# Optimization experiments

Measured on AMD Instinct MI355X. Metric: run time of the kernel, lower is better.

Reference implementation:

```python
import jax, jax.numpy as jnp
import numpy as np

B, C, H, W, NCH = 2, 256, 48, 48, 12


def setup_inputs() -> dict:
    key = jax.random.key(0)
    k1, k2, k3, k4, k5 = jax.random.split(key, 5)
    gray_feature = jax.random.normal(k1, (B, C, H, W), jnp.float32)
    rgb_feature = jax.random.normal(k2, (B, C, H, W), jnp.float32)
    rgb_image = jax.random.uniform(k3, (B, 3, H, W), jnp.float32)
    # one-hot segmentation labels: random class id per pixel in [0, NCH)
    gcls = jax.random.randint(k4, (B, H, W), 0, NCH)
    rcls = jax.random.randint(k5, (B, H, W), 0, NCH)
    gray_label = jax.nn.one_hot(gcls, NCH, axis=1, dtype=jnp.float32)
    rgb_label = jax.nn.one_hot(rcls, NCH, axis=1, dtype=jnp.float32)
    return dict(gray_feature=gray_feature, rgb_feature=rgb_feature,
                rgb_image=rgb_image, gray_label=gray_label, rgb_label=rgb_label)


def _masked_normalize(feat, maskf):
    # feat: [b,c,N], maskf: [b,N] in {0,1}. Subtract per-channel masked mean,
    # then divide each masked pixel's feature vector by its channel-norm.
    cnt = maskf.sum(-1)                                            # [b]
    mean = jnp.einsum('bcn,bn->bc', feat, maskf) / jnp.maximum(cnt, 1.0)[:, None]
    bar = (feat - mean[:, :, None]) * maskf[:, None, :]            # zero outside mask
    norm = jnp.sqrt(jnp.sum(bar * bar, axis=1))                    # [b,N]
    unit = bar / jnp.where(norm > 0, norm, 1.0)[:, None, :]
    return unit, cnt


def reference(gray_feature, rgb_feature, rgb_image, gray_label, rgb_label):
    b, c, h, w = gray_feature.shape
    N = h * w
    gf = gray_feature.reshape(b, c, N)
    rf = rgb_feature.reshape(b, c, N)
    img = rgb_image.reshape(b, 3, N)
    gms = gray_label.reshape(b, -1, N) > 0.5   # [b,NCH,N] bool
    rms = rgb_label.reshape(b, -1, N) > 0.5
    canvas = -jnp.ones((b, 3, N), gray_feature.dtype)
    NEG = jnp.asarray(-1e30, gray_feature.dtype)
    for k in range(1, 12):  # classes 1..11, matching the torch loop
        gm = gms[:, k]                                     # [b,N]
        rm = rms[:, k]
        gmf = gm.astype(gf.dtype)
        rmf = rm.astype(rf.dtype)
        gn, cg = _masked_normalize(gf, gmf)                # [b,c,N]
        rn, cr = _masked_normalize(rf, rmf)
        # normalized correlation between gray and rgb masked pixels
        corr = jnp.einsum('bci,bcj->bij', gn, rn)          # [b,N,N]
        logits = jnp.where(rm[:, None, :], corr, NEG)      # softmax over rgb-mask pixels
        sm = jax.nn.softmax(logits, axis=-1)
        out = jnp.einsum('bij,bcj->bci', sm, img)          # [b,3,N]
        # skip condition from torch: needs >=2 pixels on each side
        valid = (cg > 1) & (cr > 1)                        # [b]
        write = gm & valid[:, None]                        # [b,N]
        canvas = jnp.where(write[:, None, :], out, canvas)
    return canvas.reshape(b, 3, h, w)
```

## Files before the change

### kernel.cpp

```cpp
#include <hip/hip_runtime.h>
#include <math.h>

#define BN 2
#define CC 256
#define NN 2304
#define KK 12
#define MC 320
#define QT 16
#define KTL 256
#define KCH 32
#define BPAD 260
#define APAD 18
#define KB_ACT 11

#define OFF_CNT_G   0
#define OFF_CNT_R   32
#define OFF_IDX_G   64
#define OFF_CPS_G   (OFF_IDX_G + BN * KK * MC)
#define OFF_CPS_R   (OFF_CPS_G + BN * NN)
#define OFF_MSUM_G  (OFF_CPS_R + BN * NN)
#define OFF_MSUM_R  (OFF_MSUM_G + BN * KK * CC)
#define OFF_IMGC    (OFF_MSUM_R + BN * KK * CC)
#define OFF_INV_G   (OFF_IMGC + BN * KK * 3 * MC)
#define OFF_INV_R   (OFF_INV_G + BN * KK * MC)
#define OFF_UCG     (OFF_INV_R + BN * KK * MC)
#define OFF_UCR     (OFF_UCG + BN * KK * MC * CC)

__global__ __launch_bounds__(256) void prep_mean_kernel(
        const float* __restrict__ gf, const float* __restrict__ rf,
        const float* __restrict__ img, const float* __restrict__ gl,
        const float* __restrict__ rl, float* __restrict__ out,
        int* cnt_g, int* cnt_r, int* idx_g, int* cps_g, int* cps_r,
        float* imgc, float* inv_g, float* inv_r,
        float* msum_g, float* msum_r) {
    __shared__ int wcnt[4];
    __shared__ float wsum[4][4][KK];
    int bid = blockIdx.x, tid = threadIdx.x;
    int lane = tid & 63, wid = tid >> 6;

    if (bid < 48) {
        int type = bid / (BN * KK);
        int rem = bid % (BN * KK);
        int b = rem / KK, k = rem % KK;
        const float* lp = (type ? rl : gl) + ((size_t)(b * KK + k)) * NN;
        int* cps = type ? cps_r : cps_g;
        int* cnt = type ? cnt_r : cnt_g;
        int base = 0;
        for (int c0 = 0; c0 < NN; c0 += 256) {
            int i = c0 + tid;
            bool p = lp[i] > 0.5f;
            unsigned long long m = __ballot(p);
            int rank = __popcll(m & ((1ull << lane) - 1));
            if (lane == 0) wcnt[wid] = __popcll(m);
            __syncthreads();
            int pre = 0;
            for (int w = 0; w < wid; ++w) pre += wcnt[w];
            int tot = wcnt[0] + wcnt[1] + wcnt[2] + wcnt[3];
            if (p) {
                int pos = base + pre + rank;
                cps[b * NN + i] = (k << 16) | pos;
                if (pos < MC) {
                    if (type) {
                        for (int ch = 0; ch < 3; ++ch)
                            imgc[((b * KK + k) * 3 + ch) * MC + pos] =
                                img[((size_t)(b * 3 + ch)) * NN + i];
                    } else {
                        idx_g[(b * KK + k) * MC + pos] = i;
                    }
                }
            }
            base += tot;
            __syncthreads();
        }
        if (tid == 0) cnt[b * KK + k] = base;
        int start = base < MC ? base : MC;
        for (int pos = start + tid; pos < MC; pos += 256) {
            if (type) {
                for (int ch = 0; ch < 3; ++ch)
                    imgc[((b * KK + k) * 3 + ch) * MC + pos] = 0.f;
            } else {
                idx_g[(b * KK + k) * MC + pos] = 0;
            }
        }
        float* invc = type ? inv_r : inv_g;
        for (int pos = tid; pos < MC; pos += 256)
            invc[(b * KK + k) * MC + pos] = 0.f;
    } else {
        int u = bid - 48;
        if (u < 54) out[u * 256 + tid] = -1.0f;
        int type = u >> 7;
        int rem = u & 127;
        int b = rem >> 6, cg = rem & 63;
        const float* fb = (type ? rf : gf) + ((size_t)(b * CC + cg * 4)) * NN;
        const float* lab = (type ? rl : gl) + ((size_t)b) * KK * NN;
        float* msum = type ? msum_r : msum_g;

        float acc[4][KK];
        #pragma unroll
        for (int c = 0; c < 4; ++c)
            #pragma unroll
            for (int kk = 0; kk < KK; ++kk) acc[c][kk] = 0.f;
        for (int i = tid; i < NN; i += 256) {
            float lv[KK];
            #pragma unroll
            for (int kk = 0; kk < KK; ++kk) lv[kk] = lab[(size_t)kk * NN + i];
            #pragma unroll
            for (int c = 0; c < 4; ++c) {
                float v = fb[(size_t)c * NN + i];
                #pragma unroll
                for (int kk = 0; kk < KK; ++kk) acc[c][kk] += lv[kk] * v;
            }
        }
        #pragma unroll
        for (int c = 0; c < 4; ++c)
            #pragma unroll
            for (int kk = 0; kk < KK; ++kk) {
                #pragma unroll
                for (int o = 32; o; o >>= 1)
                    acc[c][kk] += __shfl_xor(acc[c][kk], o, 64);
            }
        if (lane == 0) {
            #pragma unroll
            for (int c = 0; c < 4; ++c)
                #pragma unroll
                for (int kk = 0; kk < KK; ++kk) wsum[wid][c][kk] = acc[c][kk];
        }
        __syncthreads();
        if (tid < 48) {
            int c = tid / KK, kk = tid % KK;
            float s = wsum[0][c][kk] + wsum[1][c][kk] + wsum[2][c][kk] + wsum[3][c][kk];
            msum[(b * KK + kk) * CC + cg * 4 + c] = s;
        }
    }
}

__global__ __launch_bounds__(256) void center_kernel(
        const float* __restrict__ gf, const float* __restrict__ rf,
        const int* __restrict__ cps_g, const int* __restrict__ cps_r,
        const int* __restrict__ cnt_g, const int* __restrict__ cnt_r,
        const float* __restrict__ msum_g, const float* __restrict__ msum_r,
        float* ucg, float* ucr, float* inv_g, float* inv_r) {
    const int PCH = NN / 32;
    int blk = blockIdx.x;
    int type = blk / (BN * PCH);
    int rem = blk % (BN * PCH);
    int b = rem / PCH, chunk = rem % PCH;
    int i0 = chunk * 32;
    const float* f = type ? rf : gf;
    const int* cps = type ? cps_r : cps_g;
    const int* cnt = type ? cnt_r : cnt_g;
    const float* msum = type ? msum_r : msum_g;
    float* uc = type ? ucr : ucg;
    float* invc = type ? inv_r : inv_g;

    __shared__ float lmean[KK * 257];
    __shared__ float tile[64 * 33];

    int tid = threadIdx.x;
    for (int x = tid; x < KK * CC; x += 256) {
        int k = x >> 8, c = x & 255;
        float cn = fmaxf((float)cnt[b * KK + k], 1.f);
        lmean[k * 257 + c] = msum[(b * KK + k) * CC + c] / cn;
    }
    int p = tid >> 3, q = tid & 7;
    int pl = tid & 31, cb = tid >> 5;
    int kcpos = cps[b * NN + i0 + p];
    int kc = kcpos >> 16, pos = kcpos & 0xFFFF;
    bool wr = pos < MC;
    float ss = 0.f;
    float* ub = uc + ((size_t)((b * KK + kc) * MC + (wr ? pos : MC - 1))) * CC;
    for (int cc = 0; cc < 4; ++cc) {
        __syncthreads();
        for (int j = 0; j < 8; ++j) {
            int c = cb * 8 + j;
            tile[c * 33 + pl] = f[((size_t)(b * CC + cc * 64 + c)) * NN + i0 + pl];
        }
        __syncthreads();
        #pragma unroll
        for (int h = 0; h < 2; ++h) {
            int c0 = q * 8 + h * 4;
            float4 v;
            v.x = tile[(c0 + 0) * 33 + p] - lmean[kc * 257 + cc * 64 + c0 + 0];
            v.y = tile[(c0 + 1) * 33 + p] - lmean[kc * 257 + cc * 64 + c0 + 1];
            v.z = tile[(c0 + 2) * 33 + p] - lmean[kc * 257 + cc * 64 + c0 + 2];
            v.w = tile[(c0 + 3) * 33 + p] - lmean[kc * 257 + cc * 64 + c0 + 3];
            ss += v.x * v.x + v.y * v.y + v.z * v.z + v.w * v.w;
            if (wr) *(float4*)&ub[cc * 64 + c0] = v;
        }
    }
    ss += __shfl_xor(ss, 1, 64);
    ss += __shfl_xor(ss, 2, 64);
    ss += __shfl_xor(ss, 4, 64);
    if (q == 0 && wr)
        invc[(b * KK + kc) * MC + pos] = (ss > 0.f) ? rsqrtf(ss) : 1.0f;
}

__global__ __launch_bounds__(512) void corr_out_kernel(
        const int* __restrict__ cnt_g, const int* __restrict__ cnt_r,
        const int* __restrict__ idx_g,
        const float* __restrict__ ucg, const float* __restrict__ ucr,
        const float* __restrict__ inv_g, const float* __restrict__ inv_r,
        const float* __restrict__ imgc, float* __restrict__ out) {
    const int TNQ = MC / QT;
    const int NWG = BN * KB_ACT * TNQ;
    int bid = blockIdx.x;
    int x = (bid & 7) * (NWG / 8) + (bid >> 3);
    int tq = x % TNQ;
    int rest = x / TNQ;
    int k = 1 + rest % KB_ACT;
    int b = rest / KB_ACT;
    int bk = b * KK + k;
    int cg_ = cnt_g[bk], cr_ = cnt_r[bk];
    if (cg_ <= 1 || cr_ <= 1) return;
    int Mg = min(cg_, MC), Mr = min(cr_, MC);
    int q0 = tq * QT;
    if (q0 >= Mg) return;
    int mrp = (Mr + 3) & ~3;

    __shared__ float Af[CC * APAD];
    __shared__ float Bs[KCH * BPAD];

    int tid = threadIdx.x;
    {
        int r = tid >> 5, c32 = tid & 31;
        int rowi = q0 + r; if (rowi > MC - 1) rowi = MC - 1;
        const float* rowA = ucg + ((size_t)(bk * MC + rowi)) * CC;
        float4 v0 = *(const float4*)&rowA[c32 * 8];
        float4 v1 = *(const float4*)&rowA[c32 * 8 + 4];
        Af[(c32 * 8 + 0) * APAD + r] = v0.x;
        Af[(c32 * 8 + 1) * APAD + r] = v0.y;
        Af[(c32 * 8 + 2) * APAD + r] = v0.z;
        Af[(c32 * 8 + 3) * APAD + r] = v0.w;
        Af[(c32 * 8 + 4) * APAD + r] = v1.x;
        Af[(c32 * 8 + 5) * APAD + r] = v1.y;
        Af[(c32 * 8 + 6) * APAD + r] = v1.z;
        Af[(c32 * 8 + 7) * APAD + r] = v1.w;
    }

    int wid = tid >> 6;
    int lane = tid & 63;
    int r0 = q0 + 2 * wid;
    int r0c = (r0 > MC - 1) ? MC - 1 : r0;
    int r1c = (r0 + 1 > MC - 1) ? MC - 1 : r0 + 1;
    float invi0 = inv_g[bk * MC + r0c];
    float invi1 = inv_g[bk * MC + r1c];
    const float* im0 = imgc + (bk * 3 + 0) * MC;
    const float* im1 = imgc + (bk * 3 + 1) * MC;
    const float* im2 = imgc + (bk * 3 + 2) * MC;
    const float* ivr = inv_r + bk * MC;
    float s[2] = {0.f, 0.f}, p0[2] = {0.f, 0.f}, p1[2] = {0.f, 0.f}, p2[2] = {0.f, 0.f};

    for (int k0 = 0; k0 < Mr; k0 += KTL) {
        float acc[2][4];
        #pragma unroll
        for (int xx = 0; xx < 2; ++xx)
            #pragma unroll
            for (int y = 0; y < 4; ++y) acc[xx][y] = 0.f;
        int lim = mrp - k0;

        for (int kcc = 0; kcc < CC; kcc += KCH) {
            __syncthreads();
            {
                int cj = tid & 7;
                int colg = tid >> 3;
                #pragma unroll
                for (int p8 = 0; p8 < 4; ++p8) {
                    int col = colg + p8 * 64;
                    if (col < lim) {
                        int colr = k0 + col; if (colr > MC - 1) colr = MC - 1;
                        float4 vb = *(const float4*)(ucr +
                            ((size_t)(bk * MC + colr)) * CC + kcc + cj * 4);
                        Bs[(cj * 4 + 0) * BPAD + col] = vb.x;
                        Bs[(cj * 4 + 1) * BPAD + col] = vb.y;
                        Bs[(cj * 4 + 2) * BPAD + col] = vb.z;
                        Bs[(cj * 4 + 3) * BPAD + col] = vb.w;
                    }
                }
            }
            __syncthreads();
            #pragma unroll
            for (int kk = 0; kk < KCH; ++kk) {
                float2 av = *(const float2*)&Af[(kcc + kk) * APAD + 2 * wid];
                float4 bv = *(const float4*)&Bs[kk * BPAD + lane * 4];
                acc[0][0] += av.x * bv.x; acc[0][1] += av.x * bv.y;
                acc[0][2] += av.x * bv.z; acc[0][3] += av.x * bv.w;
                acc[1][0] += av.y * bv.x; acc[1][1] += av.y * bv.y;
                acc[1][2] += av.y * bv.z; acc[1][3] += av.y * bv.w;
            }
        }
        int kbase = k0 + lane * 4; if (kbase > MC - 4) kbase = MC - 4;
        float4 w0 = *(const float4*)&im0[kbase];
        float4 w1 = *(const float4*)&im1[kbase];
        float4 w2 = *(const float4*)&im2[kbase];
        float4 vj = *(const float4*)&ivr[kbase];
        float wj0[4] = {w0.x, w0.y, w0.z, w0.w};
        float wj1[4] = {w1.x, w1.y, w1.z, w1.w};
        float wj2[4] = {w2.x, w2.y, w2.z, w2.w};
        float vjj[4] = {vj.x, vj.y, vj.z, vj.w};
        #pragma unroll
        for (int y = 0; y < 4; ++y) {
            int col = k0 + lane * 4 + y;
            bool ok = col < Mr;
            float e0 = ok ? __expf(acc[0][y] * invi0 * vjj[y]) : 0.f;
            float e1 = ok ? __expf(acc[1][y] * invi1 * vjj[y]) : 0.f;
            s[0] += e0; p0[0] += e0 * wj0[y]; p1[0] += e0 * wj1[y]; p2[0] += e0 * wj2[y];
            s[1] += e1; p0[1] += e1 * wj0[y]; p1[1] += e1 * wj1[y]; p2[1] += e1 * wj2[y];
        }
    }
    #pragma unroll
    for (int o = 1; o <= 32; o <<= 1) {
        #pragma unroll
        for (int xx = 0; xx < 2; ++xx) {
            s[xx]  += __shfl_xor(s[xx],  o, 64);
            p0[xx] += __shfl_xor(p0[xx], o, 64);
            p1[xx] += __shfl_xor(p1[xx], o, 64);
            p2[xx] += __shfl_xor(p2[xx], o, 64);
        }
    }
    if (lane == 0) {
        #pragma unroll
        for (int xx = 0; xx < 2; ++xx) {
            int row = q0 + 2 * wid + xx;
            if (row < Mg) {
                int gi = idx_g[bk * MC + row];
                float inv = 1.0f / s[xx];
                out[((size_t)(b * 3 + 0)) * NN + gi] = p0[xx] * inv;
                out[((size_t)(b * 3 + 1)) * NN + gi] = p1[xx] * inv;
                out[((size_t)(b * 3 + 2)) * NN + gi] = p2[xx] * inv;
            }
        }
    }
}

extern "C" void kernel_launch(void* const* d_in, const int* in_sizes, int n_in,
                              void* d_out, int out_size, void* d_ws, size_t ws_size,
                              hipStream_t stream) {
    const float* gf  = (const float*)d_in[0];
    const float* rf  = (const float*)d_in[1];
    const float* img = (const float*)d_in[2];
    const float* gl  = (const float*)d_in[3];
    const float* rl  = (const float*)d_in[4];
    float* out = (float*)d_out;
    float* ws = (float*)d_ws;

    int*   cnt_g  = (int*)(ws + OFF_CNT_G);
    int*   cnt_r  = (int*)(ws + OFF_CNT_R);
    int*   idx_g  = (int*)(ws + OFF_IDX_G);
    int*   cps_g  = (int*)(ws + OFF_CPS_G);
    int*   cps_r  = (int*)(ws + OFF_CPS_R);
    float* msum_g = ws + OFF_MSUM_G;
    float* msum_r = ws + OFF_MSUM_R;
    float* imgc   = ws + OFF_IMGC;
    float* inv_g  = ws + OFF_INV_G;
    float* inv_r  = ws + OFF_INV_R;
    float* ucg    = ws + OFF_UCG;
    float* ucr    = ws + OFF_UCR;

    prep_mean_kernel<<<48 + 2 * BN * (CC / 4), 256, 0, stream>>>(
        gf, rf, img, gl, rl, out, cnt_g, cnt_r, idx_g, cps_g, cps_r,
        imgc, inv_g, inv_r, msum_g, msum_r);
    center_kernel<<<2 * BN * (NN / 32), 256, 0, stream>>>(
        gf, rf, cps_g, cps_r, cnt_g, cnt_r, msum_g, msum_r,
        ucg, ucr, inv_g, inv_r);
    corr_out_kernel<<<BN * KB_ACT * (MC / QT), 512, 0, stream>>>(
        cnt_g, cnt_r, idx_g, ucg, ucr, inv_g, inv_r, imgc, out);
}
```

Before: 113.8 us.

## Fuse three kernels into one cooperative persistent kernel with grid syncs

Combines the prep/mean, centering and correlation-softmax kernels into a single cooperative kernel of 256 blocks of 512 threads. The blocks loop over the former jobs and use grid.sync between phases instead of separate kernel launches. This removes the launch gaps between stages. In exchange it adds grid-wide barrier cost, reduces parallelism in the correlation phase (previously 440 blocks), and changes per-job thread mappings to suit 512-thread blocks.

```diff
diff --git a/kernel.cpp b/kernel.cpp
--- a/kernel.cpp
+++ b/kernel.cpp
@@ -1,5 +1,8 @@
 #include <hip/hip_runtime.h>
+#include <hip/hip_cooperative_groups.h>
 #include <math.h>
+
+namespace cg = cooperative_groups;
 
 #define BN 2
 #define CC 256
@@ -12,6 +15,8 @@
 #define BPAD 260
 #define APAD 18
 #define KB_ACT 11
+#define GRID 256
+#define BLK 512
 
 #define OFF_CNT_G   0
 #define OFF_CNT_R   32
@@ -26,307 +31,311 @@
 #define OFF_UCG     (OFF_INV_R + BN * KK * MC)
 #define OFF_UCR     (OFF_UCG + BN * KK * MC * CC)
 
-__global__ __launch_bounds__(256) void prep_mean_kernel(
+__global__ __launch_bounds__(BLK) void fused_kernel(
         const float* __restrict__ gf, const float* __restrict__ rf,
         const float* __restrict__ img, const float* __restrict__ gl,
         const float* __restrict__ rl, float* __restrict__ out,
-        int* cnt_g, int* cnt_r, int* idx_g, int* cps_g, int* cps_r,
-        float* imgc, float* inv_g, float* inv_r,
-        float* msum_g, float* msum_r) {
-    __shared__ int wcnt[4];
-    __shared__ float wsum[4][4][KK];
-    int bid = blockIdx.x, tid = threadIdx.x;
-    int lane = tid & 63, wid = tid >> 6;
-
-    if (bid < 48) {
-        int type = bid / (BN * KK);
-        int rem = bid % (BN * KK);
-        int b = rem / KK, k = rem % KK;
-        const float* lp = (type ? rl : gl) + ((size_t)(b * KK + k)) * NN;
-        int* cps = type ? cps_r : cps_g;
-        int* cnt = type ? cnt_r : cnt_g;
-        int base = 0;
-        for (int c0 = 0; c0 < NN; c0 += 256) {
-            int i = c0 + tid;
-            bool p = lp[i] > 0.5f;
-            unsigned long long m = __ballot(p);
-            int rank = __popcll(m & ((1ull << lane) - 1));
-            if (lane == 0) wcnt[wid] = __popcll(m);
-            __syncthreads();
-            int pre = 0;
-            for (int w = 0; w < wid; ++w) pre += wcnt[w];
-            int tot = wcnt[0] + wcnt[1] + wcnt[2] + wcnt[3];
-            if (p) {
-                int pos = base + pre + rank;
-                cps[b * NN + i] = (k << 16) | pos;
-                if (pos < MC) {
+        int* __restrict__ cnt_g, int* __restrict__ cnt_r,
+        int* __restrict__ idx_g, int* __restrict__ cps_g, int* __restrict__ cps_r,
+        float* __restrict__ imgc, float* __restrict__ inv_g, float* __restrict__ inv_r,
+        float* __restrict__ msum_g, float* __restrict__ msum_r,
+        float* __restrict__ ucg, float* __restrict__ ucr) {
+    cg::grid_group grid = cg::this_grid();
+    __shared__ float smem[CC * APAD + KCH * BPAD];
+
+    const int bid = blockIdx.x, tid = threadIdx.x;
+    const int lane = tid & 63, wid = tid >> 6;
+
+    {
+        int* wcnt = (int*)smem;
+        float* wsum = smem + 8;
+        for (int job = bid; job < 48 + 2 * BN * (CC / 4); job += GRID) {
+            if (job < 48) {
+                int type = job / (BN * KK);
+                int rem = job % (BN * KK);
+                int b = rem / KK, k = rem % KK;
+                const float* lp = (type ? rl : gl) + ((size_t)(b * KK + k)) * NN;
+                int* cps = type ? cps_r : cps_g;
+                int* cnt = type ? cnt_r : cnt_g;
+                int base = 0;
+                for (int c0 = 0; c0 < NN; c0 += BLK) {
+                    int i = c0 + tid;
+                    bool p = (i < NN) && (lp[i] > 0.5f);
+                    unsigned long long m = __ballot(p);
+                    int rank = __popcll(m & ((1ull << lane) - 1));
+                    if (lane == 0) wcnt[wid] = __popcll(m);
+                    __syncthreads();
+                    int pre = 0;
+                    for (int w = 0; w < wid; ++w) pre += wcnt[w];
+                    int tot = 0;
+                    for (int w = 0; w < 8; ++w) tot += wcnt[w];
+                    if (p) {
+                        int pos = base + pre + rank;
+                        cps[b * NN + i] = (k << 16) | pos;
+                        if (pos < MC) {
+                            if (type) {
+                                for (int ch = 0; ch < 3; ++ch)
+                                    imgc[((b * KK + k) * 3 + ch) * MC + pos] =
+                                        img[((size_t)(b * 3 + ch)) * NN + i];
+                            } else {
+                                idx_g[(b * KK + k) * MC + pos] = i;
+                            }
+                        }
+                    }
+                    base += tot;
+                    __syncthreads();
+                }
+                if (tid == 0) cnt[b * KK + k] = base;
+                int start = base < MC ? base : MC;
+                for (int pos = start + tid; pos < MC; pos += BLK) {
                     if (type) {
                         for (int ch = 0; ch < 3; ++ch)
-                            imgc[((b * KK + k) * 3 + ch) * MC + pos] =
-                                img[((size_t)(b * 3 + ch)) * NN + i];
+                            imgc[((b * KK + k) * 3 + ch) * MC + pos] = 0.f;
                     } else {
-                        idx_g[(b * KK + k) * MC + pos] = i;
-                    }
-                }
-            }
-            base += tot;
-            __syncthreads();
-        }
-        if (tid == 0) cnt[b * KK + k] = base;
-        int start = base < MC ? base : MC;
-        for (int pos = start + tid; pos < MC; pos += 256) {
-            if (type) {
-                for (int ch = 0; ch < 3; ++ch)
-                    imgc[((b * KK + k) * 3 + ch) * MC + pos] = 0.f;
+                        idx_g[(b * KK + k) * MC + pos] = 0;
+                    }
+                }
+                float* invc = type ? inv_r : inv_g;
+                for (int pos = tid; pos < MC; pos += BLK)
+                    invc[(b * KK + k) * MC + pos] = 0.f;
             } else {
-                idx_g[(b * KK + k) * MC + pos] = 0;
-            }
-        }
-        float* invc = type ? inv_r : inv_g;
-        for (int pos = tid; pos < MC; pos += 256)
-            invc[(b * KK + k) * MC + pos] = 0.f;
-    } else {
-        int u = bid - 48;
-        if (u < 54) out[u * 256 + tid] = -1.0f;
-        int type = u >> 7;
-        int rem = u & 127;
-        int b = rem >> 6, cg = rem & 63;
-        const float* fb = (type ? rf : gf) + ((size_t)(b * CC + cg * 4)) * NN;
-        const float* lab = (type ? rl : gl) + ((size_t)b) * KK * NN;
-        float* msum = type ? msum_r : msum_g;
-
-        float acc[4][KK];
-        #pragma unroll
-        for (int c = 0; c < 4; ++c)
-            #pragma unroll
-            for (int kk = 0; kk < KK; ++kk) acc[c][kk] = 0.f;
-        for (int i = tid; i < NN; i += 256) {
-            float lv[KK];
-            #pragma unroll
-            for (int kk = 0; kk < KK; ++kk) lv[kk] = lab[(size_t)kk * NN + i];
-            #pragma unroll
-            for (int c = 0; c < 4; ++c) {
-                float v = fb[(size_t)c * NN + i];
-                #pragma unroll
-                for (int kk = 0; kk < KK; ++kk) acc[c][kk] += lv[kk] * v;
-            }
-        }
-        #pragma unroll
-        for (int c = 0; c < 4; ++c)
-            #pragma unroll
-            for (int kk = 0; kk < KK; ++kk) {
-                #pragma unroll
-                for (int o = 32; o; o >>= 1)
-                    acc[c][kk] += __shfl_xor(acc[c][kk], o, 64);
-            }
-        if (lane == 0) {
-            #pragma unroll
-            for (int c = 0; c < 4; ++c)
-                #pragma unroll
-                for (int kk = 0; kk < KK; ++kk) wsum[wid][c][kk] = acc[c][kk];
-        }
-        __syncthreads();
-        if (tid < 48) {
-            int c = tid / KK, kk = tid % KK;
-            float s = wsum[0][c][kk] + wsum[1][c][kk] + wsum[2][c][kk] + wsum[3][c][kk];
-            msum[(b * KK + kk) * CC + cg * 4 + c] = s;
+                int u = job - 48;
+                if (u < 27) out[u * BLK + tid] = -1.0f;
+                int type = u >> 7;
+                int rem = u & 127;
+                int b = rem >> 6, cgq = rem & 63;
+                const float* fb = (type ? rf : gf) + ((size_t)(b * CC + cgq * 4)) * NN;
+                const float* lab = (type ? rl : gl) + ((size_t)b) * KK * NN;
+                float* msum = type ? msum_r : msum_g;
+
+                float acc[4][KK];
+                #pragma unroll
+                for (int c = 0; c < 4; ++c)
+                    #pragma unroll
+                    for (int kk = 0; kk < KK; ++kk) acc[c][kk] = 0.f;
+                for (int i = tid; i < NN; i += BLK) {
+                    float lv[KK];
+                    #pragma unroll
+                    for (int kk = 0; kk < KK; ++kk) lv[kk] = lab[(size_t)kk * NN + i];
+                    #pragma unroll
+                    for (int c = 0; c < 4; ++c) {
+                        float v = fb[(size_t)c * NN + i];
+                        #pragma unroll
+                        for (int kk = 0; kk < KK; ++kk) acc[c][kk] += lv[kk] * v;
+                    }
+                }
+                #pragma unroll
+                for (int c = 0; c < 4; ++c)
+                    #pragma unroll
+                    for (int kk = 0; kk < KK; ++kk) {
+                        #pragma unroll
+                        for (int o = 32; o; o >>= 1)
+                            acc[c][kk] += __shfl_xor(acc[c][kk], o, 64);
+                    }
+                if (lane == 0) {
+                    #pragma unroll
+                    for (int c = 0; c < 4; ++c)
+                        #pragma unroll
+                        for (int kk = 0; kk < KK; ++kk)
+                            wsum[(wid * 4 + c) * KK + kk] = acc[c][kk];
+                }
+                __syncthreads();
+                if (tid < 48) {
+                    int c = tid / KK, kk = tid % KK;
+                    float s = 0.f;
+                    for (int w = 0; w < 8; ++w) s += wsum[(w * 4 + c) * KK + kk];
+                    msum[(b * KK + kk) * CC + cgq * 4 + c] = s;
+                }
+            }
         }
     }
-}
-
-__global__ __launch_bounds__(256) void center_kernel(
-        const float* __restrict__ gf, const float* __restrict__ rf,
-        const int* __restrict__ cps_g, const int* __restrict__ cps_r,
-        const int* __restrict__ cnt_g, const int* __restrict__ cnt_r,
-        const float* __restrict__ msum_g, const float* __restrict__ msum_r,
-        float* ucg, float* ucr, float* inv_g, float* inv_r) {
-    const int PCH = NN / 32;
-    int blk = blockIdx.x;
-    int type = blk / (BN * PCH);
-    int rem = blk % (BN * PCH);
-    int b = rem / PCH, chunk = rem % PCH;
-    int i0 = chunk * 32;
-    const float* f = type ? rf : gf;
-    const int* cps = type ? cps_r : cps_g;
-    const int* cnt = type ? cnt_r : cnt_g;
-    const float* msum = type ? msum_r : msum_g;
-    float* uc = type ? ucr : ucg;
-    float* invc = type ? inv_r : inv_g;
-
-    __shared__ float lmean[KK * 257];
-    __shared__ float tile[64 * 33];
-
-    int tid = threadIdx.x;
-    for (int x = tid; x < KK * CC; x += 256) {
-        int k = x >> 8, c = x & 255;
-        float cn = fmaxf((float)cnt[b * KK + k], 1.f);
-        lmean[k * 257 + c] = msum[(b * KK + k) * CC + c] / cn;
-    }
-    int p = tid >> 3, q = tid & 7;
-    int pl = tid & 31, cb = tid >> 5;
-    int kcpos = cps[b * NN + i0 + p];
-    int kc = kcpos >> 16, pos = kcpos & 0xFFFF;
-    bool wr = pos < MC;
-    float ss = 0.f;
-    float* ub = uc + ((size_t)((b * KK + kc) * MC + (wr ? pos : MC - 1))) * CC;
-    for (int cc = 0; cc < 4; ++cc) {
-        __syncthreads();
-        for (int j = 0; j < 8; ++j) {
-            int c = cb * 8 + j;
-            tile[c * 33 + pl] = f[((size_t)(b * CC + cc * 64 + c)) * NN + i0 + pl];
-        }
-        __syncthreads();
-        #pragma unroll
-        for (int h = 0; h < 2; ++h) {
-            int c0 = q * 8 + h * 4;
-            float4 v;
-            v.x = tile[(c0 + 0) * 33 + p] - lmean[kc * 257 + cc * 64 + c0 + 0];
-            v.y = tile[(c0 + 1) * 33 + p] - lmean[kc * 257 + cc * 64 + c0 + 1];
-            v.z = tile[(c0 + 2) * 33 + p] - lmean[kc * 257 + cc * 64 + c0 + 2];
-            v.w = tile[(c0 + 3) * 33 + p] - lmean[kc * 257 + cc * 64 + c0 + 3];
-            ss += v.x * v.x + v.y * v.y + v.z * v.z + v.w * v.w;
-            if (wr) *(float4*)&ub[cc * 64 + c0] = v;
+    __threadfence();
+    grid.sync();
+
+    {
+        float* lmean = smem;
+        float* tile = smem + KK * 257;
+        const int PCH = NN / 32;
+        for (int job = bid; job < 2 * BN * PCH; job += GRID) {
+            __syncthreads();
+            int type = job / (BN * PCH);
+            int rem = job % (BN * PCH);
+            int b = rem / PCH, chunk = rem % PCH;
+            int i0 = chunk * 32;
+            const float* f = type ? rf : gf;
+            const int* cps = type ? cps_r : cps_g;
+            const int* cnt = type ? cnt_r : cnt_g;
+            const float* msum = type ? msum_r : msum_g;
+            float* uc = type ? ucr : ucg;
+            float* invc = type ? inv_r : inv_g;
+
+            for (int x = tid; x < KK * CC; x += BLK) {
+                int k = x >> 8, c = x & 255;
+                float cn = fmaxf((float)cnt[b * KK + k], 1.f);
+                lmean[k * 257 + c] = msum[(b * KK + k) * CC + c] / cn;
+            }
+            int p = tid >> 4, q = tid & 15;
+            int pl = tid & 31, cb = tid >> 5;
+            int kcpos = cps[b * NN + i0 + p];
+            int kc = kcpos >> 16, pos = kcpos & 0xFFFF;
+            bool wr = pos < MC;
+            float ss = 0.f;
+            float* ub = uc + ((size_t)((b * KK + kc) * MC + (wr ? pos : MC - 1))) * CC;
+            for (int cc = 0; cc < 4; ++cc) {
+                __syncthreads();
+                #pragma unroll
+                for (int j = 0; j < 4; ++j) {
+                    int c = cb * 4 + j;
+                    tile[c * 33 + pl] = f[((size_t)(b * CC + cc * 64 + c)) * NN + i0 + pl];
+                }
+                __syncthreads();
+                int c0 = q * 4;
+                float4 v;
+                v.x = tile[(c0 + 0) * 33 + p] - lmean[kc * 257 + cc * 64 + c0 + 0];
+                v.y = tile[(c0 + 1) * 33 + p] - lmean[kc * 257 + cc * 64 + c0 + 1];
+                v.z = tile[(c0 + 2) * 33 + p] - lmean[kc * 257 + cc * 64 + c0 + 2];
+                v.w = tile[(c0 + 3) * 33 + p] - lmean[kc * 257 + cc * 64 + c0 + 3];
+                ss += v.x * v.x + v.y * v.y + v.z * v.z + v.w * v.w;
+                if (wr) *(float4*)&ub[cc * 64 + c0] = v;
+            }
+            ss += __shfl_xor(ss, 1, 64);
+            ss += __shfl_xor(ss, 2, 64);
+            ss += __shfl_xor(ss, 4, 64);
+            ss += __shfl_xor(ss, 8, 64);
+            if (q == 0 && wr)
+                invc[(b * KK + kc) * MC + pos] = (ss > 0.f) ? rsqrtf(ss) : 1.0f;
         }
     }
-    ss += __shfl_xor(ss, 1, 64);
-    ss += __shfl_xor(ss, 2, 64);
-    ss += __shfl_xor(ss, 4, 64);
-    if (q == 0 && wr)
-        invc[(b * KK + kc) * MC + pos] = (ss > 0.f) ? rsqrtf(ss) : 1.0f;
-}
-
-__global__ __launch_bounds__(512) void corr_out_kernel(
-        const int* __restrict__ cnt_g, const int* __restrict__ cnt_r,
-        const int* __restrict__ idx_g,
-        const float* __restrict__ ucg, const float* __restrict__ ucr,
-        const float* __restrict__ inv_g, const float* __restrict__ inv_r,
-        const float* __restrict__ imgc, float* __restrict__ out) {
-    const int TNQ = MC / QT;
-    const int NWG = BN * KB_ACT * TNQ;
-    int bid = blockIdx.x;
-    int x = (bid & 7) * (NWG / 8) + (bid >> 3);
-    int tq = x % TNQ;
-    int rest = x / TNQ;
-    int k = 1 + rest % KB_ACT;
-    int b = rest / KB_ACT;
-    int bk = b * KK + k;
-    int cg_ = cnt_g[bk], cr_ = cnt_r[bk];
-    if (cg_ <= 1 || cr_ <= 1) return;
-    int Mg = min(cg_, MC), Mr = min(cr_, MC);
-    int q0 = tq * QT;
-    if (q0 >= Mg) return;
-    int mrp = (Mr + 3) & ~3;
-
-    __shared__ float Af[CC * APAD];
-    __shared__ float Bs[KCH * BPAD];
-
-    int tid = threadIdx.x;
+    __threadfence();
+    grid.sync();
+
     {
-        int r = tid >> 5, c32 = tid & 31;
-        int rowi = q0 + r; if (rowi > MC - 1) rowi = MC - 1;
-        const float* rowA = ucg + ((size_t)(bk * MC + rowi)) * CC;
-        float4 v0 = *(const float4*)&rowA[c32 * 8];
-        float4 v1 = *(const float4*)&rowA[c32 * 8 + 4];
-        Af[(c32 * 8 + 0) * APAD + r] = v0.x;
-        Af[(c32 * 8 + 1) * APAD + r] = v0.y;
-        Af[(c32 * 8 + 2) * APAD + r] = v0.z;
-        Af[(c32 * 8 + 3) * APAD + r] = v0.w;
-        Af[(c32 * 8 + 4) * APAD + r] = v1.x;
-        Af[(c32 * 8 + 5) * APAD + r] = v1.y;
-        Af[(c32 * 8 + 6) * APAD + r] = v1.z;
-        Af[(c32 * 8 + 7) * APAD + r] = v1.w;
-    }
-
-    int wid = tid >> 6;
-    int lane = tid & 63;
-    int r0 = q0 + 2 * wid;
-    int r0c = (r0 > MC - 1) ? MC - 1 : r0;
-    int r1c = (r0 + 1 > MC - 1) ? MC - 1 : r0 + 1;
-    float invi0 = inv_g[bk * MC + r0c];
-    float invi1 = inv_g[bk * MC + r1c];
-    const float* im0 = imgc + (bk * 3 + 0) * MC;
-    const float* im1 = imgc + (bk * 3 + 1) * MC;
-    const float* im2 = imgc + (bk * 3 + 2) * MC;
-    const float* ivr = inv_r + bk * MC;
-    float s[2] = {0.f, 0.f}, p0[2] = {0.f, 0.f}, p1[2] = {0.f, 0.f}, p2[2] = {0.f, 0.f};
-
-    for (int k0 = 0; k0 < Mr; k0 += KTL) {
-        float acc[2][4];
-        #pragma unroll
-        for (int xx = 0; xx < 2; ++xx)
+        float* Af = smem;
+        float* Bs = smem + CC * APAD;
+        const int TNQ = MC / QT;
+        const int NWG = BN * KB_ACT * TNQ;
+        for (int job = bid; job < NWG; job += GRID) {
+            __syncthreads();
+            int x = (job & 7) * (NWG / 8) + (job >> 3);
+            int tq = x % TNQ;
+            int rest = x / TNQ;
+            int k = 1 + rest % KB_ACT;
+            int b = rest / KB_ACT;
+            int bk = b * KK + k;
+            int cg_ = cnt_g[bk], cr_ = cnt_r[bk];
+            if (cg_ <= 1 || cr_ <= 1) continue;
+            int Mg = min(cg_, MC), Mr = min(cr_, MC);
+            int q0 = tq * QT;
+            if (q0 >= Mg) continue;
+            int mrp = (Mr + 3) & ~3;
+
+            {
+                int r = tid >> 5, c32 = tid & 31;
+                int rowi = q0 + r; if (rowi > MC - 1) rowi = MC - 1;
+                const float* rowA = ucg + ((size_t)(bk * MC + rowi)) * CC;
+                float4 v0 = *(const float4*)&rowA[c32 * 8];
+                float4 v1 = *(const float4*)&rowA[c32 * 8 + 4];
+                Af[(c32 * 8 + 0) * APAD + r] = v0.x;
+                Af[(c32 * 8 + 1) * APAD + r] = v0.y;
+                Af[(c32 * 8 + 2) * APAD + r] = v0.z;
+                Af[(c32 * 8 + 3) * APAD + r] = v0.w;
+                Af[(c32 * 8 + 4) * APAD + r] = v1.x;
+                Af[(c32 * 8 + 5) * APAD + r] = v1.y;
+                Af[(c32 * 8 + 6) * APAD + r] = v1.z;
+                Af[(c32 * 8 + 7) * APAD + r] = v1.w;
+            }
+
+            int wv = tid >> 6;
+            int r0 = q0 + 2 * wv;
+            int r0c = (r0 > MC - 1) ? MC - 1 : r0;
+            int r1c = (r0 + 1 > MC - 1) ? MC - 1 : r0 + 1;
+            float invi0 = inv_g[bk * MC + r0c];
+            float invi1 = inv_g[bk * MC + r1c];
+            const float* im0 = imgc + (bk * 3 + 0) * MC;
+            const float* im1 = imgc + (bk * 3 + 1) * MC;
+            const float* im2 = imgc + (bk * 3 + 2) * MC;
+            const float* ivr = inv_r + bk * MC;
+            float s[2] = {0.f, 0.f}, p0[2] = {0.f, 0.f}, p1[2] = {0.f, 0.f}, p2[2] = {0.f, 0.f};
+
+            for (int k0 = 0; k0 < Mr; k0 += KTL) {
+                float acc[2][4];
+                #pragma unroll
+                for (int xx = 0; xx < 2; ++xx)
+                    #pragma unroll
+                    for (int y = 0; y < 4; ++y) acc[xx][y] = 0.f;
+                int lim = mrp - k0;
+
+                for (int kcc = 0; kcc < CC; kcc += KCH) {
+                    __syncthreads();
+                    {
+                        int cj = tid & 7;
+                        int colg = tid >> 3;
+                        #pragma unroll
+                        for (int p8 = 0; p8 < 4; ++p8) {
+                            int col = colg + p8 * 64;
+                            if (col < lim) {
+                                int colr = k0 + col; if (colr > MC - 1) colr = MC - 1;
+                                float4 vb = *(const float4*)(ucr +
+                                    ((size_t)(bk * MC + colr)) * CC + kcc + cj * 4);
+                                Bs[(cj * 4 + 0) * BPAD + col] = vb.x;
+                                Bs[(cj * 4 + 1) * BPAD + col] = vb.y;
+                                Bs[(cj * 4 + 2) * BPAD + col] = vb.z;
+                                Bs[(cj * 4 + 3) * BPAD + col] = vb.w;
+                            }
+                        }
+                    }
+                    __syncthreads();
+                    #pragma unroll
+                    for (int kk = 0; kk < KCH; ++kk) {
+                        float2 av = *(const float2*)&Af[(kcc + kk) * APAD + 2 * wv];
+                        float4 bv = *(const float4*)&Bs[kk * BPAD + lane * 4];
+                        acc[0][0] += av.x * bv.x; acc[0][1] += av.x * bv.y;
+                        acc[0][2] += av.x * bv.z; acc[0][3] += av.x * bv.w;
+                        acc[1][0] += av.y * bv.x; acc[1][1] += av.y * bv.y;
+                        acc[1][2] += av.y * bv.z; acc[1][3] += av.y * bv.w;
+                    }
+                }
+                int kbase = k0 + lane * 4; if (kbase > MC - 4) kbase = MC - 4;
+                float4 w0 = *(const float4*)&im0[kbase];
+                float4 w1 = *(const float4*)&im1[kbase];
+                float4 w2 = *(const float4*)&im2[kbase];
+                float4 vj = *(const float4*)&ivr[kbase];
+                float wj0[4] = {w0.x, w0.y, w0.z, w0.w};
+                float wj1[4] = {w1.x, w1.y, w1.z, w1.w};
+                float wj2[4] = {w2.x, w2.y, w2.z, w2.w};
+                float vjj[4] = {vj.x, vj.y, vj.z, vj.w};
+                #pragma unroll
+                for (int y = 0; y < 4; ++y) {
+                    int col = k0 + lane * 4 + y;
+                    bool ok = col < Mr;
+                    float e0 = ok ? __expf(acc[0][y] * invi0 * vjj[y]) : 0.f;
+                    float e1 = ok ? __expf(acc[1][y] * invi1 * vjj[y]) : 0.f;
+                    s[0] += e0; p0[0] += e0 * wj0[y]; p1[0] += e0 * wj1[y]; p2[0] += e0 * wj2[y];
+                    s[1] += e1; p0[1] += e1 * wj0[y]; p1[1] += e1 * wj1[y]; p2[1] += e1 * wj2[y];
+                }
+            }
             #pragma unroll
-            for (int y = 0; y < 4; ++y) acc[xx][y] = 0.f;
-        int lim = mrp - k0;
-
-        for (int kcc = 0; kcc < CC; kcc += KCH) {
-            __syncthreads();
-            {
-                int cj = tid & 7;
-                int colg = tid >> 3;
-                #pragma unroll
-                for (int p8 = 0; p8 < 4; ++p8) {
-                    int col = colg + p8 * 64;
-                    if (col < lim) {
-                        int colr = k0 + col; if (colr > MC - 1) colr = MC - 1;
-                        float4 vb = *(const float4*)(ucr +
-                            ((size_t)(bk * MC + colr)) * CC + kcc + cj * 4);
-                        Bs[(cj * 4 + 0) * BPAD + col] = vb.x;
-                        Bs[(cj * 4 + 1) * BPAD + col] = vb.y;
-                        Bs[(cj * 4 + 2) * BPAD + col] = vb.z;
-                        Bs[(cj * 4 + 3) * BPAD + col] = vb.w;
-                    }
-                }
-            }
-            __syncthreads();
-            #pragma unroll
-            for (int kk = 0; kk < KCH; ++kk) {
-                float2 av = *(const float2*)&Af[(kcc + kk) * APAD + 2 * wid];
-                float4 bv = *(const float4*)&Bs[kk * BPAD + lane * 4];
-                acc[0][0] += av.x * bv.x; acc[0][1] += av.x * bv.y;
-                acc[0][2] += av.x * bv.z; acc[0][3] += av.x * bv.w;
-                acc[1][0] += av.y * bv.x; acc[1][1] += av.y * bv.y;
-                acc[1][2] += av.y * bv.z; acc[1][3] += av.y * bv.w;
-            }
-        }
-        int kbase = k0 + lane * 4; if (kbase > MC - 4) kbase = MC - 4;
-        float4 w0 = *(const float4*)&im0[kbase];
-        float4 w1 = *(const float4*)&im1[kbase];
-        float4 w2 = *(const float4*)&im2[kbase];
-        float4 vj = *(const float4*)&ivr[kbase];
-        float wj0[4] = {w0.x, w0.y, w0.z, w0.w};
-        float wj1[4] = {w1.x, w1.y, w1.z, w1.w};
-        float wj2[4] = {w2.x, w2.y, w2.z, w2.w};
-        float vjj[4] = {vj.x, vj.y, vj.z, vj.w};
-        #pragma unroll
-        for (int y = 0; y < 4; ++y) {
-            int col = k0 + lane * 4 + y;
-            bool ok = col < Mr;
-            float e0 = ok ? __expf(acc[0][y] * invi0 * vjj[y]) : 0.f;
-            float e1 = ok ? __expf(acc[1][y] * invi1 * vjj[y]) : 0.f;
-            s[0] += e0; p0[0] += e0 * wj0[y]; p1[0] += e0 * wj1[y]; p2[0] += e0 * wj2[y];
-            s[1] += e1; p0[1] += e1 * wj0[y]; p1[1] += e1 * wj1[y]; p2[1] += e1 * wj2[y];
-        }
-    }
-    #pragma unroll
-    for (int o = 1; o <= 32; o <<= 1) {
-        #pragma unroll
-        for (int xx = 0; xx < 2; ++xx) {
-            s[xx]  += __shfl_xor(s[xx],  o, 64);
-            p0[xx] += __shfl_xor(p0[xx], o, 64);
-            p1[xx] += __shfl_xor(p1[xx], o, 64);
-            p2[xx] += __shfl_xor(p2[xx], o, 64);
-        }
-    }
-    if (lane == 0) {
-        #pragma unroll
-        for (int xx = 0; xx < 2; ++xx) {
-            int row = q0 + 2 * wid + xx;
-            if (row < Mg) {
-                int gi = idx_g[bk * MC + row];
-                float inv = 1.0f / s[xx];
-                out[((size_t)(b * 3 + 0)) * NN + gi] = p0[xx] * inv;
-                out[((size_t)(b * 3 + 1)) * NN + gi] = p1[xx] * inv;
-                out[((size_t)(b * 3 + 2)) * NN + gi] = p2[xx] * inv;
+            for (int o = 1; o <= 32; o <<= 1) {
+                #pragma unroll
+                for (int xx = 0; xx < 2; ++xx) {
+                    s[xx]  += __shfl_xor(s[xx],  o, 64);
+                    p0[xx] += __shfl_xor(p0[xx], o, 64);
+                    p1[xx] += __shfl_xor(p1[xx], o, 64);
+                    p2[xx] += __shfl_xor(p2[xx], o, 64);
+                }
+            }
+            if (lane == 0) {
+                #pragma unroll
+                for (int xx = 0; xx < 2; ++xx) {
+                    int row = q0 + 2 * wv + xx;
+                    if (row < Mg) {
+                        int gi = idx_g[bk * MC + row];
+                        float inv = 1.0f / s[xx];
+                        out[((size_t)(b * 3 + 0)) * NN + gi] = p0[xx] * inv;
+                        out[((size_t)(b * 3 + 1)) * NN + gi] = p1[xx] * inv;
+                        out[((size_t)(b * 3 + 2)) * NN + gi] = p2[xx] * inv;
+                    }
+                }
             }
         }
     }
@@ -356,12 +365,9 @@
     float* ucg    = ws + OFF_UCG;
     float* ucr    = ws + OFF_UCR;
 
-    prep_mean_kernel<<<48 + 2 * BN * (CC / 4), 256, 0, stream>>>(
-        gf, rf, img, gl, rl, out, cnt_g, cnt_r, idx_g, cps_g, cps_r,
-        imgc, inv_g, inv_r, msum_g, msum_r);
-    center_kernel<<<2 * BN * (NN / 32), 256, 0, stream>>>(
-        gf, rf, cps_g, cps_r, cnt_g, cnt_r, msum_g, msum_r,
-        ucg, ucr, inv_g, inv_r);
-    corr_out_kernel<<<BN * KB_ACT * (MC / QT), 512, 0, stream>>>(
-        cnt_g, cnt_r, idx_g, ucg, ucr, inv_g, inv_r, imgc, out);
+    void* args[] = {&gf, &rf, &img, &gl, &rl, &out,
+                    &cnt_g, &cnt_r, &idx_g, &cps_g, &cps_r,
+                    &imgc, &inv_g, &inv_r, &msum_g, &msum_r, &ucg, &ucr};
+    hipLaunchCooperativeKernel((void*)fused_kernel, dim3(GRID), dim3(BLK),
+                               args, 0, stream);
 }
```

Result: slower. 284.8 us (+150.3%).
